# Kernel tuning notes

Measured on AMD Instinct MI355X. Metric: run time of the kernel, lower is better.

Reference implementation:

```python
import jax, jax.numpy as jnp
import numpy as np

HID = 1024
HEADS = 16
HEAD_DIM = HID // HEADS
INTER = 4 * HID
EPS = 1e-6
SCALE = 1.0 / np.sqrt(HEAD_DIM)


def setup_inputs() -> dict:
    key = jax.random.key(0)
    ks = jax.random.split(key, 8)
    s = 0.02
    return {
        "x": jax.random.normal(ks[0], (2, 2048, HID), dtype=jnp.float32),
        "wq": jax.random.normal(ks[1], (HID, HID), dtype=jnp.float32) * s,
        "wk": jax.random.normal(ks[2], (HID, HID), dtype=jnp.float32) * s,
        "wv": jax.random.normal(ks[3], (HID, HID), dtype=jnp.float32) * s,
        "wo": jax.random.normal(ks[4], (HID, HID), dtype=jnp.float32) * s,
        "w_gate": jax.random.normal(ks[5], (INTER, HID), dtype=jnp.float32) * s,
        "w_up": jax.random.normal(ks[6], (INTER, HID), dtype=jnp.float32) * s,
        "w_down": jax.random.normal(ks[7], (HID, INTER), dtype=jnp.float32) * s,
        "norm1_w": jnp.ones((HID,), dtype=jnp.float32),
        "norm2_w": jnp.ones((HID,), dtype=jnp.float32),
    }


def _rmsnorm(x, w):
    rms = jnp.sqrt(jnp.mean(x * x, axis=-1, keepdims=True) + EPS)
    return x / rms * w


def reference(x, wq, wk, wv, wo, w_gate, w_up, w_down, norm1_w, norm2_w):
    b, s, _ = x.shape
    residual = x
    h = _rmsnorm(x, norm1_w)
    # projections: nn.Linear computes h @ W.T
    q = (h @ wq.T).reshape(b, s, HEADS, HEAD_DIM).transpose(0, 2, 1, 3)
    k = (h @ wk.T).reshape(b, s, HEADS, HEAD_DIM).transpose(0, 2, 1, 3)
    v = (h @ wv.T).reshape(b, s, HEADS, HEAD_DIM).transpose(0, 2, 1, 3)
    scores = jnp.einsum("bhqd,bhkd->bhqk", q, k) * SCALE
    attn = jax.nn.softmax(scores, axis=-1)
    out = jnp.einsum("bhqk,bhkd->bhqd", attn, v)
    out = out.transpose(0, 2, 1, 3).reshape(b, s, HID)
    x = residual + out @ wo.T
    residual = x
    h = _rmsnorm(x, norm2_w)
    gate = jax.nn.silu(h @ w_gate.T)
    up = h @ w_up.T
    mlp_out = (gate * up) @ w_down.T
    return residual + mlp_out
```

## Files before the change

kernel.cpp:

```cpp
#include <hip/hip_runtime.h>
#include <hip/hip_bf16.h>

#define HID 1024
#define SEQ 2048
#define NTOK 4096
#define ATT_SCALE 0.125f

typedef __attribute__((ext_vector_type(4))) float f32x4;
typedef __attribute__((ext_vector_type(16))) float f32x16;
typedef __attribute__((ext_vector_type(8))) __bf16 bf16x8;
typedef __attribute__((ext_vector_type(4))) __bf16 bf16x4;
typedef __bf16 bf16;

__device__ __forceinline__ bf16 f2bf(float f) { return (bf16)f; }

__device__ __forceinline__ void gld_lds16(const void* g, void* l) {
  __builtin_amdgcn_global_load_lds((const __attribute__((address_space(1))) void*)g,
                                   (__attribute__((address_space(3))) void*)l,
                                   16, 0, 0);
}

__device__ __forceinline__ f32x4 mfma16(bf16x8 a, bf16x8 b, f32x4 c) {
  return __builtin_amdgcn_mfma_f32_16x16x32_bf16(a, b, c, 0, 0, 0);
}
__device__ __forceinline__ f32x16 mfma32(bf16x8 a, bf16x8 b, f32x16 c) {
  return __builtin_amdgcn_mfma_f32_32x32x16_bf16(a, b, c, 0, 0, 0);
}

struct CvtArgs {
  const float* src[7];
  bf16* dst[7];
};

__global__ __launch_bounds__(256) void cvt_weights(CvtArgs a) {
  const int g = blockIdx.x * 256 + threadIdx.x;
  const int s = g >> 18;
  const int seg = s < 4 ? s : (s < 8 ? 4 : (s < 12 ? 5 : 6));
  const int start = seg < 4 ? (seg << 18) : (((seg - 4) << 20) + (1 << 20));
  const int loc = (g - start) << 2;
  const float4 v = *(const float4*)(a.src[seg] + loc);
  bf16x4 o = {f2bf(v.x), f2bf(v.y), f2bf(v.z), f2bf(v.w)};
  *(bf16x4*)(a.dst[seg] + loc) = o;
}

__global__ __launch_bounds__(256) void rmsnorm_k(const float* __restrict__ x,
                                                 const float* __restrict__ w,
                                                 bf16* __restrict__ h) {
  const int row = blockIdx.x;
  const int tid = threadIdx.x;
  const float4 xv = *(const float4*)(x + (size_t)row * HID + tid * 4);
  float ss = xv.x * xv.x + xv.y * xv.y + xv.z * xv.z + xv.w * xv.w;
#pragma unroll
  for (int m = 1; m < 64; m <<= 1) ss += __shfl_xor(ss, m, 64);
  __shared__ float wsum[4];
  if ((tid & 63) == 0) wsum[tid >> 6] = ss;
  __syncthreads();
  const float tot = wsum[0] + wsum[1] + wsum[2] + wsum[3];
  const float inv = rsqrtf(tot * (1.0f / HID) + 1e-6f);
  const float4 wv = *(const float4*)(w + tid * 4);
  bf16x4 o = {f2bf(xv.x * inv * wv.x), f2bf(xv.y * inv * wv.y),
              f2bf(xv.z * inv * wv.z), f2bf(xv.w * inv * wv.w)};
  *(bf16x4*)(h + (size_t)row * HID + tid * 4) = o;
}

__global__ __launch_bounds__(512, 2) void gemm256(const bf16* __restrict__ A,
                                                  const bf16* __restrict__ B,
                                                  bf16* __restrict__ C,
                                                  int N, int K) {
  alignas(16) __shared__ bf16 As[2][256][64];
  alignas(16) __shared__ bf16 Bs[2][256][64];
  const int tid = threadIdx.x;
  const int wid = tid >> 6, lane = tid & 63;
  const int wm = wid >> 2, wn = wid & 3;
  const int bm0 = blockIdx.y << 8, bn0 = blockIdx.x << 8;

  const int srow = (wid << 3) + (lane >> 3);
  const int gch = ((lane & 7) ^ (lane >> 3)) << 3;
  const bf16* gA = A + (size_t)(bm0 + srow) * K + gch;
  const bf16* gB = B + (size_t)(bn0 + srow) * K + gch;

  const int fr = lane & 15, fc = lane >> 4, fx = lane & 7;

  f32x4 acc[8][4] = {};
  const int nt = K >> 6;

  auto stage = [&](int c, int k0) {
#pragma unroll
    for (int i = 0; i < 4; ++i)
      gld_lds16(gA + (size_t)(i * 64) * K + k0, &As[c][i * 64 + (wid << 3)][0]);
#pragma unroll
    for (int i = 0; i < 4; ++i)
      gld_lds16(gB + (size_t)(i * 64) * K + k0, &Bs[c][i * 64 + (wid << 3)][0]);
  };

  stage(0, 0);
  stage(1, 64);
  asm volatile("s_waitcnt vmcnt(8)" ::: "memory");
  __builtin_amdgcn_s_barrier();
  __builtin_amdgcn_sched_barrier(0);

  for (int t = 0; t < nt; ++t) {
    const int c = t & 1;
    bf16x8 bfrag[2][4];
#pragma unroll
    for (int s = 0; s < 2; ++s)
#pragma unroll
      for (int n = 0; n < 4; ++n)
        bfrag[s][n] = *(const bf16x8*)&Bs[c][wn * 64 + n * 16 + fr]
                                         [(((s << 2) + fc) ^ fx) << 3];
#pragma unroll
    for (int q = 0; q < 4; ++q) {
      bf16x8 af[2][2];
#pragma unroll
      for (int mi = 0; mi < 2; ++mi)
#pragma unroll
        for (int s = 0; s < 2; ++s)
          af[mi][s] = *(const bf16x8*)&As[c][wm * 128 + (q * 2 + mi) * 16 + fr]
                                           [(((s << 2) + fc) ^ fx) << 3];
      __builtin_amdgcn_s_setprio(1);
#pragma unroll
      for (int mi = 0; mi < 2; ++mi)
#pragma unroll
        for (int n = 0; n < 4; ++n)
#pragma unroll
          for (int s = 0; s < 2; ++s)
            acc[q * 2 + mi][n] = mfma16(af[mi][s], bfrag[s][n], acc[q * 2 + mi][n]);
      __builtin_amdgcn_s_setprio(0);
    }
    __builtin_amdgcn_sched_barrier(0);
    __builtin_amdgcn_s_barrier();
    __builtin_amdgcn_sched_barrier(0);
    if (t + 2 < nt) {
      stage(c, (t + 2) << 6);
      asm volatile("s_waitcnt vmcnt(8)" ::: "memory");
    } else {
      asm volatile("s_waitcnt vmcnt(0)" ::: "memory");
    }
    __builtin_amdgcn_s_barrier();
    __builtin_amdgcn_sched_barrier(0);
  }

#pragma unroll
  for (int m = 0; m < 8; ++m) {
    const int row = bm0 + wm * 128 + m * 16 + (fc << 2);
#pragma unroll
    for (int n = 0; n < 4; ++n) {
      const int col = bn0 + wn * 64 + n * 16 + fr;
#pragma unroll
      for (int r = 0; r < 4; ++r)
        C[(size_t)(row + r) * N + col] = f2bf(acc[m][n][r]);
    }
  }
}

template <int EPI>
__global__ __launch_bounds__(256) void gemm_bt(const bf16* __restrict__ A, int lda,
                                               const bf16* __restrict__ B, int ldb,
                                               void* __restrict__ C,
                                               const float* __restrict__ R,
                                               int ldc, int K) {
  alignas(16) __shared__ bf16 As[128 * 32];
  alignas(16) __shared__ bf16 Bs[128 * 32];
  const int tid = threadIdx.x;
  const int wid = tid >> 6;
  const int lane = tid & 63;
  const int bm0 = blockIdx.y * 128;
  const int bn0 = blockIdx.x * 128;
  const int wr = wid >> 1, wc = wid & 1;

  f32x4 acc[4][4] = {};

  const int sr = tid >> 2;
  const int sc = (tid & 3) << 3;
  const bf16* gA = A + (size_t)(bm0 + sr) * lda + sc;
  const bf16* gB = B + (size_t)(bn0 + sr) * ldb + sc;
  bf16* lA = As + wid * 512;
  bf16* lB = Bs + wid * 512;
  const int frow = lane & 15;
  const int kofs = (lane >> 4) << 3;

  for (int k0 = 0; k0 < K; k0 += 32) {
    __syncthreads();
    gld_lds16(gA + k0, lA);
    gld_lds16(gA + k0 + (size_t)64 * lda, lA + 2048);
    gld_lds16(gB + k0, lB);
    gld_lds16(gB + k0 + (size_t)64 * ldb, lB + 2048);
    __syncthreads();
    bf16x8 af[4], bfr[4];
#pragma unroll
    for (int m = 0; m < 4; ++m)
      af[m] = *(const bf16x8*)(As + (wr * 64 + m * 16 + frow) * 32 + kofs);
#pragma unroll
    for (int n = 0; n < 4; ++n)
      bfr[n] = *(const bf16x8*)(Bs + (wc * 64 + n * 16 + frow) * 32 + kofs);
#pragma unroll
    for (int m = 0; m < 4; ++m)
#pragma unroll
      for (int n = 0; n < 4; ++n)
        acc[m][n] = mfma16(af[m], bfr[n], acc[m][n]);
  }

  const int er = bm0 + wr * 64 + ((lane >> 4) << 2);
  const int ec = bn0 + wc * 64 + (lane & 15);
#pragma unroll
  for (int m = 0; m < 4; ++m)
#pragma unroll
    for (int n = 0; n < 4; ++n)
#pragma unroll
      for (int r = 0; r < 4; ++r) {
        const size_t idx = (size_t)(er + m * 16 + r) * ldc + (ec + n * 16);
        if (EPI == 0) ((bf16*)C)[idx] = f2bf(acc[m][n][r]);
        else          ((float*)C)[idx] = R[idx] + acc[m][n][r];
      }
}

__global__ __launch_bounds__(256) void vtrans_k(const bf16* __restrict__ qkv,
                                                bf16* __restrict__ vt) {
  const int bh = blockIdx.y;
  const int b = bh >> 4, head = bh & 15;
  const int st0 = blockIdx.x * 64;
  const int wid = threadIdx.x >> 6, lane = threadIdx.x & 63;
  const bf16* src = qkv + ((size_t)b * SEQ + st0 + lane) * 3072 + 2 * HID + head * 64 + wid * 16;
  bf16* dst = vt + (size_t)bh * (64 * SEQ) + st0 + lane;
#pragma unroll
  for (int half = 0; half < 2; ++half) {
    bf16x8 v = *(const bf16x8*)(src + half * 8);
#pragma unroll
    for (int i = 0; i < 8; ++i)
      dst[(size_t)(wid * 16 + half * 8 + i) * SEQ] = v[i];
  }
}

__global__ __launch_bounds__(128) void attn_k(const bf16* __restrict__ qkv,
                                              const bf16* __restrict__ vt,
                                              bf16* __restrict__ attn_out) {
  const int bh = blockIdx.y;
  const int b = bh >> 4, head = bh & 15;
  const int tid = threadIdx.x, wid = tid >> 6, lane = tid & 63;
  const int l31 = lane & 31, h = lane >> 5;
  const int r7 = l31 & 7;

  alignas(16) __shared__ bf16 Ks[64 * 64];
  alignas(16) __shared__ bf16 Vs[64 * 64];

  const size_t tokq = (size_t)b * SEQ + blockIdx.x * 64 + wid * 32 + l31;
  bf16x8 qf[4];
#pragma unroll
  for (int s = 0; s < 4; ++s) {
    bf16x8 t = *(const bf16x8*)(qkv + tokq * 3072 + head * 64 + s * 16 + h * 8);
#pragma unroll
    for (int i = 0; i < 8; ++i) t[i] = f2bf((float)t[i] * ATT_SCALE);
    qf[s] = t;
  }

  const int sr = tid >> 1;
  const int sc = (tid & 1) * 32;
  const int p5 = sr & 31;
  const int keyr = (sr & 32) | (p5 & 16) | (((p5 >> 2) & 1) << 3) | (((p5 >> 3) & 1) << 2) | (p5 & 3);
  const bf16* kg = qkv + ((size_t)b * SEQ + keyr) * 3072 + HID + head * 64 + sc;
  const bf16* vg = vt + (size_t)bh * (64 * SEQ) + (size_t)sr * SEQ + sc;
  int wofs[4];
#pragma unroll
  for (int j = 0; j < 4; ++j)
    wofs[j] = sr * 64 + ((((sc >> 3) + j) ^ (sr & 7)) << 3);

  f32x16 o0 = {}, o1 = {};
  float m = -1e30f, l = 0.f;

  for (int t0 = 0; t0 < SEQ; t0 += 64) {
    __syncthreads();
#pragma unroll
    for (int j = 0; j < 4; ++j) {
      bf16x8 kv = *(const bf16x8*)(kg + (size_t)t0 * 3072 + j * 8);
      *(bf16x8*)(Ks + wofs[j]) = kv;
      bf16x8 vv = *(const bf16x8*)(vg + t0 + j * 8);
      *(bf16x8*)(Vs + wofs[j]) = vv;
    }
    __syncthreads();

    f32x16 s0 = {}, s1 = {};
#pragma unroll
    for (int s = 0; s < 4; ++s) {
      bf16x8 k0 = *(const bf16x8*)(Ks + l31 * 64 + (((2 * s + h) ^ r7) << 3));
      s0 = mfma32(k0, qf[s], s0);
      bf16x8 k1 = *(const bf16x8*)(Ks + (32 + l31) * 64 + (((2 * s + h) ^ r7) << 3));
      s1 = mfma32(k1, qf[s], s1);
    }

    float pmax = s0[0];
#pragma unroll
    for (int i = 1; i < 16; ++i) pmax = fmaxf(pmax, s0[i]);
#pragma unroll
    for (int i = 0; i < 16; ++i) pmax = fmaxf(pmax, s1[i]);
    pmax = fmaxf(pmax, __shfl_xor(pmax, 32, 64));
    const float mnew = fmaxf(m, pmax);
    const float al = __expf(m - mnew);
    m = mnew;

    bf16x8 pa[4];
    float sum = 0.f;
#pragma unroll
    for (int t = 0; t < 2; ++t)
#pragma unroll
      for (int j = 0; j < 8; ++j) {
        const float p = __expf(s0[8 * t + j] - mnew);
        sum += p;
        pa[t][j] = f2bf(p);
      }
#pragma unroll
    for (int t = 0; t < 2; ++t)
#pragma unroll
      for (int j = 0; j < 8; ++j) {
        const float p = __expf(s1[8 * t + j] - mnew);
        sum += p;
        pa[2 + t][j] = f2bf(p);
      }
    sum += __shfl_xor(sum, 32, 64);
    l = l * al + sum;
#pragma unroll
    for (int i = 0; i < 16; ++i) { o0[i] *= al; o1[i] *= al; }

#pragma unroll
    for (int t = 0; t < 4; ++t) {
      bf16x8 v0 = *(const bf16x8*)(Vs + l31 * 64 + (((2 * t + h) ^ r7) << 3));
      o0 = mfma32(v0, pa[t], o0);
      bf16x8 v1 = *(const bf16x8*)(Vs + (32 + l31) * 64 + (((2 * t + h) ^ r7) << 3));
      o1 = mfma32(v1, pa[t], o1);
    }
  }

  const float inv = 1.0f / l;
  bf16* obase = attn_out + tokq * HID + head * 64;
#pragma unroll
  for (int rq = 0; rq < 4; ++rq) {
    bf16x4 w0, w1;
#pragma unroll
    for (int i = 0; i < 4; ++i) {
      w0[i] = f2bf(o0[4 * rq + i] * inv);
      w1[i] = f2bf(o1[4 * rq + i] * inv);
    }
    *(bf16x4*)(obase + 8 * rq + 4 * h) = w0;
    *(bf16x4*)(obase + 32 + 8 * rq + 4 * h) = w1;
  }
}

__global__ __launch_bounds__(256) void silu_mul_k(bf16* __restrict__ gu) {
  const int t = blockIdx.x * 256 + threadIdx.x;
  const int row = t >> 9;
  const int j = (t & 511) << 3;
  bf16* p = gu + (size_t)row * 8192 + j;
  bf16x8 g8 = *(const bf16x8*)p;
  bf16x8 u8 = *(const bf16x8*)(p + 4096);
  bf16x8 o;
#pragma unroll
  for (int i = 0; i < 8; ++i) {
    const float g = (float)g8[i], u = (float)u8[i];
    const float s = g / (1.0f + __expf(-g));
    o[i] = f2bf(s * u);
  }
  *(bf16x8*)p = o;
}

extern "C" void kernel_launch(void* const* d_in, const int* in_sizes, int n_in,
                              void* d_out, int out_size, void* d_ws, size_t ws_size,
                              hipStream_t stream) {
  const float* x  = (const float*)d_in[0];
  const float* wq = (const float*)d_in[1];
  const float* wk = (const float*)d_in[2];
  const float* wv = (const float*)d_in[3];
  const float* wo = (const float*)d_in[4];
  const float* wg = (const float*)d_in[5];
  const float* wu = (const float*)d_in[6];
  const float* wd = (const float*)d_in[7];
  const float* n1 = (const float*)d_in[8];
  const float* n2 = (const float*)d_in[9];

  char* ws = (char*)d_ws;
  bf16* wqkv_b  = (bf16*)(ws);
  bf16* wo_b    = (bf16*)(ws + 6291456);
  bf16* wgu_b   = (bf16*)(ws + 8388608);
  bf16* wd_b    = (bf16*)(ws + 25165824);
  bf16* h       = (bf16*)(ws + 33554432);
  bf16* attnout = (bf16*)(ws + 41943040);
  bf16* qkv     = (bf16*)(ws + 50331648);
  bf16* vt      = (bf16*)(ws + 75497472);
  bf16* gu      = (bf16*)(ws + 50331648);
  float* x2     = (float*)d_out;

  CvtArgs ca;
  ca.src[0] = wq; ca.dst[0] = wqkv_b;
  ca.src[1] = wk; ca.dst[1] = wqkv_b + 1048576;
  ca.src[2] = wv; ca.dst[2] = wqkv_b + 2097152;
  ca.src[3] = wo; ca.dst[3] = wo_b;
  ca.src[4] = wg; ca.dst[4] = wgu_b;
  ca.src[5] = wu; ca.dst[5] = wgu_b + 4194304;
  ca.src[6] = wd; ca.dst[6] = wd_b;

  cvt_weights<<<dim3(16384), dim3(256), 0, stream>>>(ca);
  rmsnorm_k<<<dim3(NTOK), dim3(256), 0, stream>>>(x, n1, h);
  gemm256<<<dim3(12, 16), dim3(512), 0, stream>>>(h, wqkv_b, qkv, 3072, 1024);
  vtrans_k<<<dim3(32, 32), dim3(256), 0, stream>>>(qkv, vt);
  attn_k<<<dim3(32, 32), dim3(128), 0, stream>>>(qkv, vt, attnout);
  gemm_bt<1><<<dim3(8, 32), dim3(256), 0, stream>>>(attnout, 1024, wo_b, 1024,
                                                    (void*)x2, x, 1024, 1024);
  rmsnorm_k<<<dim3(NTOK), dim3(256), 0, stream>>>(x2, n2, h);
  gemm256<<<dim3(32, 16), dim3(512), 0, stream>>>(h, wgu_b, gu, 8192, 1024);
  silu_mul_k<<<dim3(8192), dim3(256), 0, stream>>>(gu);
  gemm_bt<1><<<dim3(8, 32), dim3(256), 0, stream>>>(gu, 8192, wd_b, 4096,
                                                    (void*)d_out, (const float*)x2, 1024, 4096);
}
```

Before: 460.0 us.

## Split-K the output and down-projection GEMMs and fuse reduction into rmsnorm

The wo and w_down projections now run as split-K GEMMs with two K-halves along gridDim.z. Each half writes fp32 partials into workspace buffers, which doubles the block count from 256 to 512 to better fill the CUs. The partials are summed with the residual inside a new rmsnorm kernel (attention path) or a new add3 kernel (MLP path). This adds extra fp32 partial-buffer traffic and one extra kernel launch, and reuses workspace regions (weights and h) that are dead by then.

```diff
diff --git a/kernel.cpp b/kernel.cpp
--- a/kernel.cpp
+++ b/kernel.cpp
@@ -61,6 +61,53 @@
   bf16x4 o = {f2bf(xv.x * inv * wv.x), f2bf(xv.y * inv * wv.y),
               f2bf(xv.z * inv * wv.z), f2bf(xv.w * inv * wv.w)};
   *(bf16x4*)(h + (size_t)row * HID + tid * 4) = o;
+}
+
+__global__ __launch_bounds__(256) void rmsnorm_red_k(const float* __restrict__ x,
+                                                     const float* __restrict__ p0,
+                                                     const float* __restrict__ p1,
+                                                     const float* __restrict__ w,
+                                                     float* __restrict__ x2,
+                                                     bf16* __restrict__ h) {
+  const int row = blockIdx.x;
+  const int tid = threadIdx.x;
+  const size_t off = (size_t)row * HID + tid * 4;
+  const float4 xa = *(const float4*)(x + off);
+  const float4 pa = *(const float4*)(p0 + off);
+  const float4 pb = *(const float4*)(p1 + off);
+  float4 xv;
+  xv.x = xa.x + pa.x + pb.x;
+  xv.y = xa.y + pa.y + pb.y;
+  xv.z = xa.z + pa.z + pb.z;
+  xv.w = xa.w + pa.w + pb.w;
+  *(float4*)(x2 + off) = xv;
+  float ss = xv.x * xv.x + xv.y * xv.y + xv.z * xv.z + xv.w * xv.w;
+#pragma unroll
+  for (int m = 1; m < 64; m <<= 1) ss += __shfl_xor(ss, m, 64);
+  __shared__ float wsum[4];
+  if ((tid & 63) == 0) wsum[tid >> 6] = ss;
+  __syncthreads();
+  const float tot = wsum[0] + wsum[1] + wsum[2] + wsum[3];
+  const float inv = rsqrtf(tot * (1.0f / HID) + 1e-6f);
+  const float4 wv = *(const float4*)(w + tid * 4);
+  bf16x4 o = {f2bf(xv.x * inv * wv.x), f2bf(xv.y * inv * wv.y),
+              f2bf(xv.z * inv * wv.z), f2bf(xv.w * inv * wv.w)};
+  *(bf16x4*)(h + off) = o;
+}
+
+__global__ __launch_bounds__(256) void add3_k(float* __restrict__ out,
+                                              const float* __restrict__ p0,
+                                              const float* __restrict__ p1) {
+  const size_t i = ((size_t)blockIdx.x * 256 + threadIdx.x) * 4;
+  const float4 a = *(const float4*)(out + i);
+  const float4 b = *(const float4*)(p0 + i);
+  const float4 c = *(const float4*)(p1 + i);
+  float4 o;
+  o.x = a.x + b.x + c.x;
+  o.y = a.y + b.y + c.y;
+  o.z = a.z + b.z + c.z;
+  o.w = a.w + b.w + c.w;
+  *(float4*)(out + i) = o;
 }
 
 __global__ __launch_bounds__(512, 2) void gemm256(const bf16* __restrict__ A,
@@ -167,13 +214,14 @@
   const int bm0 = blockIdx.y * 128;
   const int bn0 = blockIdx.x * 128;
   const int wr = wid >> 1, wc = wid & 1;
+  const size_t koff = (size_t)blockIdx.z * K;
 
   f32x4 acc[4][4] = {};
 
   const int sr = tid >> 2;
   const int sc = (tid & 3) << 3;
-  const bf16* gA = A + (size_t)(bm0 + sr) * lda + sc;
-  const bf16* gB = B + (size_t)(bn0 + sr) * ldb + sc;
+  const bf16* gA = A + (size_t)(bm0 + sr) * lda + sc + koff;
+  const bf16* gB = B + (size_t)(bn0 + sr) * ldb + sc + koff;
   bf16* lA = As + wid * 512;
   bf16* lB = Bs + wid * 512;
   const int frow = lane & 15;
@@ -200,6 +248,7 @@
         acc[m][n] = mfma16(af[m], bfr[n], acc[m][n]);
   }
 
+  float* P = (EPI == 2) ? (blockIdx.z ? (float*)R : (float*)C) : nullptr;
   const int er = bm0 + wr * 64 + ((lane >> 4) << 2);
   const int ec = bn0 + wc * 64 + (lane & 15);
 #pragma unroll
@@ -209,8 +258,9 @@
 #pragma unroll
       for (int r = 0; r < 4; ++r) {
         const size_t idx = (size_t)(er + m * 16 + r) * ldc + (ec + n * 16);
-        if (EPI == 0) ((bf16*)C)[idx] = f2bf(acc[m][n][r]);
-        else          ((float*)C)[idx] = R[idx] + acc[m][n][r];
+        if (EPI == 0)      ((bf16*)C)[idx] = f2bf(acc[m][n][r]);
+        else if (EPI == 1) ((float*)C)[idx] = R[idx] + acc[m][n][r];
+        else               P[idx] = acc[m][n][r];
       }
 }
 
@@ -387,6 +437,11 @@
   bf16* gu      = (bf16*)(ws + 50331648);
   float* x2     = (float*)d_out;
 
+  float* pw0 = (float*)(ws + 50331648);
+  float* pw1 = (float*)(ws + 67108864);
+  float* pd0 = (float*)(ws);
+  float* pd1 = (float*)(ws + 33554432);
+
   CvtArgs ca;
   ca.src[0] = wq; ca.dst[0] = wqkv_b;
   ca.src[1] = wk; ca.dst[1] = wqkv_b + 1048576;
@@ -401,11 +456,12 @@
   gemm256<<<dim3(12, 16), dim3(512), 0, stream>>>(h, wqkv_b, qkv, 3072, 1024);
   vtrans_k<<<dim3(32, 32), dim3(256), 0, stream>>>(qkv, vt);
   attn_k<<<dim3(32, 32), dim3(128), 0, stream>>>(qkv, vt, attnout);
-  gemm_bt<1><<<dim3(8, 32), dim3(256), 0, stream>>>(attnout, 1024, wo_b, 1024,
-                                                    (void*)x2, x, 1024, 1024);
-  rmsnorm_k<<<dim3(NTOK), dim3(256), 0, stream>>>(x2, n2, h);
+  gemm_bt<2><<<dim3(8, 32, 2), dim3(256), 0, stream>>>(attnout, 1024, wo_b, 1024,
+                                                       (void*)pw0, (const float*)pw1, 1024, 512);
+  rmsnorm_red_k<<<dim3(NTOK), dim3(256), 0, stream>>>(x, pw0, pw1, n2, x2, h);
   gemm256<<<dim3(32, 16), dim3(512), 0, stream>>>(h, wgu_b, gu, 8192, 1024);
   silu_mul_k<<<dim3(8192), dim3(256), 0, stream>>>(gu);
-  gemm_bt<1><<<dim3(8, 32), dim3(256), 0, stream>>>(gu, 8192, wd_b, 4096,
-                                                    (void*)d_out, (const float*)x2, 1024, 4096);
-}
+  gemm_bt<2><<<dim3(8, 32, 2), dim3(256), 0, stream>>>(gu, 8192, wd_b, 4096,
+                                                       (void*)pd0, (const float*)pd1, 1024, 2048);
+  add3_k<<<dim3(4096), dim3(256), 0, stream>>>(x2, pd0, pd1);
+}
```

After: 440.9 us. 1.04x faster.
